# Optimization experiments

Hardware: AMD Instinct MI355X
Metric: run time of the kernel (lower is better)

## Reference

```python
import jax, jax.numpy as jnp
import numpy as np

B, S, D, H = 2, 2048, 1024, 16
HD = D // H
SCALE = HD ** -0.5
EPS = 1e-5


def setup_inputs() -> dict:
    key = jax.random.key(0)
    ks = jax.random.split(key, 12)
    s = 1.0 / np.sqrt(D)
    return {
        "query": jax.random.normal(ks[0], (B, S, D), jnp.float32),
        "key_": jax.random.normal(ks[1], (B, S, D), jnp.float32),
        "value": jax.random.normal(ks[2], (B, S, D), jnp.float32),
        "Wq": jax.random.normal(ks[3], (D, D), jnp.float32) * s,
        "bq": jnp.zeros((D,), jnp.float32),
        "Wk": jax.random.normal(ks[4], (D, D), jnp.float32) * s,
        "bk": jnp.zeros((D,), jnp.float32),
        "Wv": jax.random.normal(ks[5], (D, D), jnp.float32) * s,
        "bv": jnp.zeros((D,), jnp.float32),
        "Wo": jax.random.normal(ks[6], (D, D), jnp.float32) * s,
        "bo": jnp.zeros((D,), jnp.float32),
        "gamma": jnp.ones((D,), jnp.float32),
        "beta": jnp.zeros((D,), jnp.float32),
    }


def _split_heads(x):
    # [B,S,D] -> [B,H,S,HD]
    return x.reshape(B, S, H, HD).transpose(0, 2, 1, 3)


def reference(query, key_, value, Wq, bq, Wk, bk, Wv, bv, Wo, bo, gamma, beta):
    q = _split_heads(query @ Wq + bq)
    k = _split_heads(key_ @ Wk + bk)
    v = _split_heads(value @ Wv + bv)
    # [B,H,S,S] attention scores
    scores = jnp.einsum("bhqd,bhkd->bhqk", q, k) * SCALE
    probs = jax.nn.softmax(scores, axis=-1)  # dropout is identity in eval
    attn = jnp.einsum("bhqk,bhkd->bhqd", probs, v)
    attn = attn.transpose(0, 2, 1, 3).reshape(B, S, D)
    attn = attn @ Wo + bo
    # residual + LayerNorm
    x = query + attn
    mu = jnp.mean(x, axis=-1, keepdims=True)
    var = jnp.mean(jnp.square(x - mu), axis=-1, keepdims=True)
    out = (x - mu) * jax.lax.rsqrt(var + EPS) * gamma + beta
    return out
```

## Files before the change

kernel.cpp:

```cpp
#include <hip/hip_runtime.h>
#include <hip/hip_bf16.h>

#define DEVI __device__ __forceinline__

constexpr int Bb  = 2;
constexpr int Ss  = 2048;
constexpr int Dd  = 1024;
constexpr int Hh  = 16;
constexpr int HDh = 64;
constexpr int Mr  = Bb * Ss;
constexpr float kEps = 1e-5f;
constexpr float kQScale = 0.18033688011112043f;

typedef unsigned short u16;
typedef unsigned int   u32;
typedef u16 u16x8 __attribute__((ext_vector_type(8)));
typedef u16 u16x4 __attribute__((ext_vector_type(4)));
typedef __attribute__((ext_vector_type(8)))  short s16x8;
typedef __attribute__((ext_vector_type(16))) float f32x16;
typedef __attribute__((ext_vector_type(4)))  u32   u32x4;

DEVI float bf2f(u16 u) {
  return __builtin_bit_cast(float, ((unsigned int)u) << 16);
}
DEVI u16 f2bf(float f) {
  unsigned int x = __builtin_bit_cast(unsigned int, f);
  return (u16)((x + 0x7FFFu + ((x >> 16) & 1u)) >> 16);
}
DEVI u32 cvt_pk_bf16(float a, float b) {
  u32 r;
  asm("v_cvt_pk_bf16_f32 %0, %1, %2" : "=v"(r) : "v"(a), "v"(b));
  return r;
}
DEVI float vexp2(float x) {
  float r;
  asm("v_exp_f32 %0, %1" : "=v"(r) : "v"(x));
  return r;
}

DEVI void gload_lds16(const void* g, void* l) {
  __builtin_amdgcn_global_load_lds(
      (const __attribute__((address_space(1))) unsigned int*)(unsigned long long)(size_t)g,
      (__attribute__((address_space(3))) unsigned int*)(unsigned int)(size_t)l,
      16, 0, 0);
}


__global__ __launch_bounds__(256) void pack_all_fm(
    const float* __restrict__ X0, const float* __restrict__ X1,
    const float* __restrict__ X2,
    const float* __restrict__ W0, const float* __restrict__ W1,
    const float* __restrict__ W2, const float* __restrict__ W3,
    u16* __restrict__ Y0, u16* __restrict__ Y1, u16* __restrict__ Y2,
    u16* __restrict__ WfmBase) {
  __shared__ u16 Tl[64 * 64];
  const int t   = threadIdx.x;
  const int gid = blockIdx.x;
  if (gid < 3072) {
    const int z   = gid >> 10;
    const int rem = gid & 1023;
    const int r0  = (rem >> 4) * 64, k0 = (rem & 15) * 64;
    const float* X = z == 0 ? X0 : z == 1 ? X1 : X2;
    u16*         Y = z == 0 ? Y0 : z == 1 ? Y1 : Y2;
#pragma unroll
    for (int i = 0; i < 4; ++i) {
      const int idx = t + i * 256;
      const int r = idx >> 4, c4 = (idx & 15) << 2;
      const float4 v = *(const float4*)(X + (size_t)(r0 + r) * 1024 + k0 + c4);
      u16x4 p;
      p[0] = f2bf(v.x); p[1] = f2bf(v.y); p[2] = f2bf(v.z); p[3] = f2bf(v.w);
      *(u16x4*)&Tl[r * 64 + (c4 ^ (8 * (r & 7)))] = p;
    }
    __syncthreads();
#pragma unroll
    for (int i = 0; i < 2; ++i) {
      const int slot = t + i * 256;
      const int f = slot >> 6, l = slot & 63;
      const int l31 = l & 31, g2 = l >> 5;
      const int r = (f >> 2) * 32 + l31;
      const int c = (f & 3) * 16 + g2 * 8;
      const u16x8 v = *(const u16x8*)&Tl[r * 64 + (c ^ (8 * (r & 7)))];
      const size_t t32 = (size_t)(r0 >> 5) + (f >> 2);
      const int s = (k0 >> 4) + (f & 3);
      *(u16x8*)(Y + (t32 * 64 + s) * 512 + l * 8) = v;
    }
  } else {
    const int wz  = (gid - 3072) >> 8;
    const int rem = (gid - 3072) & 255;
    const int n0  = (rem >> 4) * 64, k0 = (rem & 15) * 64;
    const float* W = wz == 0 ? W0 : wz == 1 ? W1 : wz == 2 ? W2 : W3;
    u16* out = WfmBase + (size_t)wz * 1024 * 1024;
#pragma unroll
    for (int i = 0; i < 4; ++i) {
      const int idx = t + i * 256;
      const int r = idx >> 4, c4 = (idx & 15) << 2;
      const float4 v = *(const float4*)(W + (size_t)(k0 + r) * 1024 + n0 + c4);
      u16x4 p;
      p[0] = f2bf(v.x); p[1] = f2bf(v.y); p[2] = f2bf(v.z); p[3] = f2bf(v.w);
      *(u16x4*)&Tl[r * 64 + (c4 ^ (8 * (r & 7)))] = p;
    }
    __syncthreads();
#pragma unroll
    for (int i = 0; i < 2; ++i) {
      const int slot = t + i * 256;
      const int f = slot >> 6, l = slot & 63;
      const int l31 = l & 31, g2 = l >> 5;
      const int rbase = (f & 3) * 16 + g2 * 8;
      const int c = (f >> 2) * 32 + l31;
      u16x8 o;
#pragma unroll
      for (int j = 0; j < 8; ++j) {
        const int r = rbase + j;
        o[j] = Tl[r * 64 + (((c & ~3) ^ (8 * (r & 7))) | (c & 3))];
      }
      const size_t n32 = (size_t)(n0 >> 5) + (f >> 2);
      const int s = (k0 >> 4) + (f & 3);
      *(u16x8*)(out + (n32 * 64 + s) * 512 + l * 8) = o;
    }
  }
}

template <int MODE>
__global__ __launch_bounds__(256, 2) void gemm_reg_k(
    const u16* __restrict__ A0, const u16* __restrict__ A1,
    const u16* __restrict__ Wt0, const u16* __restrict__ Wt1,
    const float* b0, const float* b1, void* C0, void* C1,
    float e0, float e1) {
  constexpr int K = 1024, N = 1024;
  const int z = blockIdx.z;
  const u16*   A    = z ? A1 : A0;
  const u16*   Wt   = z ? Wt1 : Wt0;
  const float* bias = z ? b1 : b0;
  void*        Cv   = z ? C1 : C0;
  const float  esc  = z ? e1 : e0;

  const int t = threadIdx.x;
  const int lane = t & 63, w = t >> 6;
  const int l31 = lane & 31, g2 = lane >> 5;
  const int id  = blockIdx.y * 8 + blockIdx.x;
  const int sid = (id & 7) * 32 + (id >> 3);
  const int m0 = (sid >> 3) * 128, n0 = (sid & 7) * 128;
  const int wr = w >> 1, wc = w & 1;

  const u16* a0p = A  + ((size_t)(m0 >> 5) + 2 * wr) * 32768 + lane * 8;
  const u16* a1p = a0p + 32768;
  const u16* w0p = Wt + ((size_t)(n0 >> 5) + 2 * wc) * 32768 + lane * 8;
  const u16* w1p = w0p + 32768;

  f32x16 acc00, acc01, acc10, acc11;
#pragma unroll
  for (int r = 0; r < 16; ++r) { acc00[r] = 0.f; acc01[r] = 0.f; acc10[r] = 0.f; acc11[r] = 0.f; }

  s16x8 X[8], Y[8], Z[8];
  auto loadset = [&](s16x8* R, int k0) {
    const int o = (k0 >> 4) * 512;
    R[0] = *(const s16x8*)(a0p + o);  R[1] = *(const s16x8*)(a0p + o + 512);
    R[2] = *(const s16x8*)(a1p + o);  R[3] = *(const s16x8*)(a1p + o + 512);
    R[4] = *(const s16x8*)(w0p + o);  R[5] = *(const s16x8*)(w0p + o + 512);
    R[6] = *(const s16x8*)(w1p + o);  R[7] = *(const s16x8*)(w1p + o + 512);
  };
  auto compute = [&](const s16x8* R) {
#pragma unroll
    for (int s = 0; s < 2; ++s) {
      if constexpr (MODE == 1) {
        acc00 = __builtin_amdgcn_mfma_f32_32x32x16_bf16(R[0 + s], R[4 + s], acc00, 0, 0, 0);
        acc01 = __builtin_amdgcn_mfma_f32_32x32x16_bf16(R[0 + s], R[6 + s], acc01, 0, 0, 0);
        acc10 = __builtin_amdgcn_mfma_f32_32x32x16_bf16(R[2 + s], R[4 + s], acc10, 0, 0, 0);
        acc11 = __builtin_amdgcn_mfma_f32_32x32x16_bf16(R[2 + s], R[6 + s], acc11, 0, 0, 0);
      } else {
        acc00 = __builtin_amdgcn_mfma_f32_32x32x16_bf16(R[4 + s], R[0 + s], acc00, 0, 0, 0);
        acc01 = __builtin_amdgcn_mfma_f32_32x32x16_bf16(R[4 + s], R[2 + s], acc01, 0, 0, 0);
        acc10 = __builtin_amdgcn_mfma_f32_32x32x16_bf16(R[6 + s], R[0 + s], acc10, 0, 0, 0);
        acc11 = __builtin_amdgcn_mfma_f32_32x32x16_bf16(R[6 + s], R[2 + s], acc11, 0, 0, 0);
      }
    }
  };

  loadset(X, 0); loadset(Y, 32); loadset(Z, 64);
  int k = 0;
  for (int it = 0; it < 9; ++it, k += 96) {
    compute(X); loadset(X, k + 96);
    compute(Y); loadset(Y, k + 128);
    compute(Z); loadset(Z, k + 160);
  }
  compute(X); loadset(X, 960);
  compute(Y); loadset(Y, 992);
  compute(Z);
  compute(X);
  compute(Y);

  if constexpr (MODE == 1) {
    auto storeV = [&](const f32x16& a, int i, int j) {
      const int n = n0 + (2 * wc + j) * 32 + l31;
      const float bn = bias[n];
      u16* vout = (u16*)Cv + ((size_t)(m0 >> 11)) * (1024 * 2048) + (size_t)n * 2048 +
                  (m0 & 2047) + (2 * wr + i) * 32;
#pragma unroll
      for (int c = 0; c < 4; ++c) {
        u16x4 o;
#pragma unroll
        for (int rr = 0; rr < 4; ++rr) o[rr] = f2bf(a[4 * c + rr] + bn);
        *(u16x4*)(vout + 8 * c + 4 * g2) = o;
      }
    };
    storeV(acc00, 0, 0); storeV(acc01, 0, 1); storeV(acc10, 1, 0); storeV(acc11, 1, 1);
  } else {
    auto storeNM = [&](const f32x16& a, int i, int j) {
      const int m = m0 + (2 * wr + j) * 32 + l31;
#pragma unroll
      for (int c = 0; c < 4; ++c) {
        const int nb = n0 + (2 * wc + i) * 32 + 8 * c + 4 * g2;
        const float4 b4 = *(const float4*)&bias[nb];
        u16x4 o;
        o[0] = f2bf((a[4 * c + 0] + b4.x) * esc); o[1] = f2bf((a[4 * c + 1] + b4.y) * esc);
        o[2] = f2bf((a[4 * c + 2] + b4.z) * esc); o[3] = f2bf((a[4 * c + 3] + b4.w) * esc);
        *(u16x4*)((u16*)Cv + (size_t)m * N + nb) = o;
      }
    };
    storeNM(acc00, 0, 0); storeNM(acc01, 0, 1); storeNM(acc10, 1, 0); storeNM(acc11, 1, 1);
  }
}

__global__ __launch_bounds__(256, 2) void flash_mfma_k(
    const u16* __restrict__ Qb, const u16* __restrict__ Kb,
    const u16* __restrict__ Vtg, u16* __restrict__ Ofm) {
  __shared__ u16 smem[24576];
  const int t    = threadIdx.x;
  const int lane = t & 63;
  const int w    = t >> 6;
  const int l31  = lane & 31, g2 = lane >> 5;
  const int hid = (blockIdx.z * 16 + blockIdx.y) * 16 + blockIdx.x;
  const int sid = (hid & 7) * 64 + (hid >> 3);
  const int h = (sid >> 4) & 15, b = sid >> 8;
  const int q0 = (sid & 15) * 128 + w * 32;

  s16x8 qf0, qf1, qf2, qf3;
  {
    const u16* qp = Qb + ((size_t)(b * Ss + q0 + l31)) * Dd + h * HDh + 8 * g2;
    qf0 = *(const s16x8*)(qp);
    qf1 = *(const s16x8*)(qp + 16);
    qf2 = *(const s16x8*)(qp + 32);
    qf3 = *(const s16x8*)(qp + 48);
  }

  f32x16 accO0, accO1, zacc;
#pragma unroll
  for (int r = 0; r < 16; ++r) { accO0[r] = 0.f; accO1[r] = 0.f; zacc[r] = 0.f; }
  float l_run = 0.f;

  const int f0 = 2 * w, f1 = 2 * w + 1;
  const u16* kg0 = Kb + ((size_t)(b * Ss + 32 * (f0 >> 2) + l31)) * Dd + h * HDh + 16 * (f0 & 3) + 8 * g2;
  const u16* kg1 = Kb + ((size_t)(b * Ss + 32 * (f1 >> 2) + l31)) * Dd + h * HDh + 16 * (f1 & 3) + 8 * g2;
  const u16* vg0 = Vtg + ((size_t)((b * Hh + h) * HDh + 32 * (f0 >> 2) + l31)) * Ss + 16 * (f0 & 3) + 8 * g2;
  const u16* vg1 = Vtg + ((size_t)((b * Hh + h) * HDh + 32 * (f1 >> 2) + l31)) * Ss + 16 * (f1 & 3) + 8 * g2;

  auto stage = [&](int buf, int kt) {
    u16* base = &smem[buf * 8192];
    gload_lds16(kg0 + (size_t)kt * 64 * Dd, base + f0 * 512);
    gload_lds16(kg1 + (size_t)kt * 64 * Dd, base + f1 * 512);
    gload_lds16(vg0 + kt * 64, base + 4096 + f0 * 512);
    gload_lds16(vg1 + kt * 64, base + 4096 + f1 * 512);
  };

  stage(0, 0);
  stage(1, 1);

  int bi = 0;
  for (int i = 0; i < 32; ++i) {
    if (i < 31) asm volatile("s_waitcnt vmcnt(4)" ::: "memory");
    else        asm volatile("s_waitcnt vmcnt(0)" ::: "memory");
    __builtin_amdgcn_s_barrier();
    if (i + 2 < 32) {
      int sbuf = bi + 2; if (sbuf >= 3) sbuf -= 3;
      stage(sbuf, i + 2);
    }
    const u16* sb = &smem[bi * 8192];
    const int lb = lane * 8;

    f32x16 sc0, sc1;
    __builtin_amdgcn_s_setprio(1);
    {
      s16x8 ka;
      ka  = *(const s16x8*)&sb[(0 * 4 + 0) * 512 + lb];
      sc0 = __builtin_amdgcn_mfma_f32_32x32x16_bf16(ka, qf0, zacc, 0, 0, 0);
      ka  = *(const s16x8*)&sb[(0 * 4 + 1) * 512 + lb];
      sc0 = __builtin_amdgcn_mfma_f32_32x32x16_bf16(ka, qf1, sc0, 0, 0, 0);
      ka  = *(const s16x8*)&sb[(0 * 4 + 2) * 512 + lb];
      sc0 = __builtin_amdgcn_mfma_f32_32x32x16_bf16(ka, qf2, sc0, 0, 0, 0);
      ka  = *(const s16x8*)&sb[(0 * 4 + 3) * 512 + lb];
      sc0 = __builtin_amdgcn_mfma_f32_32x32x16_bf16(ka, qf3, sc0, 0, 0, 0);
    }
    __builtin_amdgcn_s_setprio(0);

    float lp = 0.f;
    u32 pw0[4][2];
#pragma unroll
    for (int c = 0; c < 4; ++c) {
      const float e0 = vexp2(sc0[4 * c + 0]);
      const float e1 = vexp2(sc0[4 * c + 1]);
      const float e2 = vexp2(sc0[4 * c + 2]);
      const float e3 = vexp2(sc0[4 * c + 3]);
      lp += (e0 + e1) + (e2 + e3);
      pw0[c][0] = cvt_pk_bf16(e0, e1);
      pw0[c][1] = cvt_pk_bf16(e2, e3);
    }

    __builtin_amdgcn_s_setprio(1);
    {
      s16x8 kb2;
      kb2 = *(const s16x8*)&sb[(1 * 4 + 0) * 512 + lb];
      sc1 = __builtin_amdgcn_mfma_f32_32x32x16_bf16(kb2, qf0, zacc, 0, 0, 0);
      kb2 = *(const s16x8*)&sb[(1 * 4 + 1) * 512 + lb];
      sc1 = __builtin_amdgcn_mfma_f32_32x32x16_bf16(kb2, qf1, sc1, 0, 0, 0);
      kb2 = *(const s16x8*)&sb[(1 * 4 + 2) * 512 + lb];
      sc1 = __builtin_amdgcn_mfma_f32_32x32x16_bf16(kb2, qf2, sc1, 0, 0, 0);
      kb2 = *(const s16x8*)&sb[(1 * 4 + 3) * 512 + lb];
      sc1 = __builtin_amdgcn_mfma_f32_32x32x16_bf16(kb2, qf3, sc1, 0, 0, 0);
    }
    __builtin_amdgcn_s_setprio(0);

#pragma unroll
    for (int s = 0; s < 2; ++s) {
      const int cb = 2 * (s & 1);
      u32 A0w = pw0[cb][0], B0w = pw0[cb + 1][0];
      u32 A1w = pw0[cb][1], B1w = pw0[cb + 1][1];
      asm("v_permlane32_swap_b32 %0, %1" : "+v"(A0w), "+v"(B0w));
      asm("v_permlane32_swap_b32 %0, %1" : "+v"(A1w), "+v"(B1w));
      u32x4 pv;
      pv[0] = A0w; pv[1] = A1w; pv[2] = B0w; pv[3] = B1w;
      const s16x8 pf = __builtin_bit_cast(s16x8, pv);
      const s16x8 v0 = *(const s16x8*)&sb[4096 + (0 * 4 + s) * 512 + lb];
      const s16x8 v1 = *(const s16x8*)&sb[4096 + (1 * 4 + s) * 512 + lb];
      __builtin_amdgcn_s_setprio(1);
      accO0 = __builtin_amdgcn_mfma_f32_32x32x16_bf16(v0, pf, accO0, 0, 0, 0);
      accO1 = __builtin_amdgcn_mfma_f32_32x32x16_bf16(v1, pf, accO1, 0, 0, 0);
      __builtin_amdgcn_s_setprio(0);
    }

    u32 pw1[4][2];
#pragma unroll
    for (int c = 0; c < 4; ++c) {
      const float e0 = vexp2(sc1[4 * c + 0]);
      const float e1 = vexp2(sc1[4 * c + 1]);
      const float e2 = vexp2(sc1[4 * c + 2]);
      const float e3 = vexp2(sc1[4 * c + 3]);
      lp += (e0 + e1) + (e2 + e3);
      pw1[c][0] = cvt_pk_bf16(e0, e1);
      pw1[c][1] = cvt_pk_bf16(e2, e3);
    }
    l_run += lp;

#pragma unroll
    for (int s = 2; s < 4; ++s) {
      const int cb = 2 * (s & 1);
      u32 A0w = pw1[cb][0], B0w = pw1[cb + 1][0];
      u32 A1w = pw1[cb][1], B1w = pw1[cb + 1][1];
      asm("v_permlane32_swap_b32 %0, %1" : "+v"(A0w), "+v"(B0w));
      asm("v_permlane32_swap_b32 %0, %1" : "+v"(A1w), "+v"(B1w));
      u32x4 pv;
      pv[0] = A0w; pv[1] = A1w; pv[2] = B0w; pv[3] = B1w;
      const s16x8 pf = __builtin_bit_cast(s16x8, pv);
      const s16x8 v0 = *(const s16x8*)&sb[4096 + (0 * 4 + s) * 512 + lb];
      const s16x8 v1 = *(const s16x8*)&sb[4096 + (1 * 4 + s) * 512 + lb];
      __builtin_amdgcn_s_setprio(1);
      accO0 = __builtin_amdgcn_mfma_f32_32x32x16_bf16(v0, pf, accO0, 0, 0, 0);
      accO1 = __builtin_amdgcn_mfma_f32_32x32x16_bf16(v1, pf, accO1, 0, 0, 0);
      __builtin_amdgcn_s_setprio(0);
    }

    bi = (bi == 2) ? 0 : bi + 1;
  }

  __syncthreads();

  const float l_tot = l_run + __shfl_xor(l_run, 32);
  const float inv = 1.f / l_tot;
  u16* Ol = &smem[w * 2304];
#pragma unroll
  for (int c = 0; c < 4; ++c) {
    u16x4 pk;
#pragma unroll
    for (int rr = 0; rr < 4; ++rr) pk[rr] = f2bf(accO0[4 * c + rr] * inv);
    *(u16x4*)&Ol[l31 * 72 + 0 * 32 + c * 8 + g2 * 4] = pk;
#pragma unroll
    for (int rr = 0; rr < 4; ++rr) pk[rr] = f2bf(accO1[4 * c + rr] * inv);
    *(u16x4*)&Ol[l31 * 72 + 1 * 32 + c * 8 + g2 * 4] = pk;
  }
  const size_t m32 = (size_t)((b * Ss + q0) >> 5);
#pragma unroll
  for (int s = 0; s < 4; ++s) {
    const u16x8 vv = *(const u16x8*)&Ol[l31 * 72 + s * 16 + g2 * 8];
    *(u16x8*)(Ofm + (m32 * 64 + h * 4 + s) * 512 + lane * 8) = vv;
  }
}

__global__ __launch_bounds__(256) void resid_ln_k(const float* __restrict__ x0,
                                                  const u16* __restrict__ x1,
                                                  const float* __restrict__ gamma,
                                                  const float* __restrict__ beta,
                                                  float* __restrict__ out) {
  const int row = blockIdx.x;
  const int t   = threadIdx.x;
  const size_t base = (size_t)row * Dd + t * 4;
  const float4 a = *(const float4*)(x0 + base);
  const u16x4  c = *(const u16x4*)(x1 + base);
  float x[4] = {a.x + bf2f(c[0]), a.y + bf2f(c[1]), a.z + bf2f(c[2]), a.w + bf2f(c[3])};
  float s  = (x[0] + x[1]) + (x[2] + x[3]);
  float s2 = fmaf(x[0], x[0], fmaf(x[1], x[1], fmaf(x[2], x[2], x[3] * x[3])));
#pragma unroll
  for (int m = 1; m < 64; m <<= 1) {
    s  += __shfl_xor(s, m);
    s2 += __shfl_xor(s2, m);
  }
  __shared__ float red[8];
  const int wave = t >> 6;
  if ((t & 63) == 0) {
    red[wave]     = s;
    red[wave + 4] = s2;
  }
  __syncthreads();
  s  = (red[0] + red[1]) + (red[2] + red[3]);
  s2 = (red[4] + red[5]) + (red[6] + red[7]);
  const float mu  = s * (1.f / Dd);
  const float var = s2 * (1.f / Dd) - mu * mu;
  const float rs  = rsqrtf(var + kEps);
  const float4 g  = *(const float4*)(gamma + t * 4);
  const float4 be = *(const float4*)(beta + t * 4);
  float4 o;
  o.x = (x[0] - mu) * rs * g.x + be.x;
  o.y = (x[1] - mu) * rs * g.y + be.y;
  o.z = (x[2] - mu) * rs * g.z + be.z;
  o.w = (x[3] - mu) * rs * g.w + be.w;
  *(float4*)(out + base) = o;
}

extern "C" void kernel_launch(void* const* d_in, const int* in_sizes, int n_in,
                              void* d_out, int out_size, void* d_ws,
                              size_t ws_size, hipStream_t stream) {
  const float* query = (const float*)d_in[0];
  const float* key_  = (const float*)d_in[1];
  const float* value = (const float*)d_in[2];
  const float* Wq = (const float*)d_in[3];
  const float* bq = (const float*)d_in[4];
  const float* Wk = (const float*)d_in[5];
  const float* bk = (const float*)d_in[6];
  const float* Wv = (const float*)d_in[7];
  const float* bv = (const float*)d_in[8];
  const float* Wo = (const float*)d_in[9];
  const float* bo = (const float*)d_in[10];
  const float* gamma = (const float*)d_in[11];
  const float* beta  = (const float*)d_in[12];
  float* out = (float*)d_out;

  char* ws = (char*)d_ws;
  u16* Xv  = (u16*)(ws + (size_t)0);
  u16* Qb  = (u16*)(ws + (size_t)0);
  u16* Kb  = (u16*)(ws + (size_t)8 * 1024 * 1024);
  u16* XoB = (u16*)(ws + (size_t)8 * 1024 * 1024);
  u16* Vtg = (u16*)(ws + (size_t)16 * 1024 * 1024);
  u16* WfB = (u16*)(ws + (size_t)24 * 1024 * 1024);
  u16* Wqf = WfB;
  u16* Wkf = WfB + (size_t)1 * 1024 * 1024;
  u16* Wvf = WfB + (size_t)2 * 1024 * 1024;
  u16* Wof = WfB + (size_t)3 * 1024 * 1024;
  u16* Xq  = (u16*)d_out;
  u16* Xk  = (u16*)d_out + (size_t)Mr * Dd;
  u16* Ofm = (u16*)d_out;

  pack_all_fm<<<4096, 256, 0, stream>>>(query, key_, value, Wq, Wk, Wv, Wo,
                                        Xq, Xk, Xv, WfB);
  gemm_reg_k<1><<<dim3(8, 32, 1), 256, 0, stream>>>(
      Xv, Xv, Wvf, Wvf, bv, bv, Vtg, Vtg, 1.f, 1.f);
  gemm_reg_k<0><<<dim3(8, 32, 2), 256, 0, stream>>>(
      Xq, Xk, Wqf, Wkf, bq, bk, Qb, Kb, kQScale, 1.f);
  flash_mfma_k<<<dim3(16, 16, 2), 256, 0, stream>>>(Qb, Kb, Vtg, Ofm);
  gemm_reg_k<0><<<dim3(8, 32, 1), 256, 0, stream>>>(
      Ofm, Ofm, Wof, Wof, bo, bo, XoB, XoB, 1.f, 1.f);
  resid_ln_k<<<Mr, 256, 0, stream>>>(query, XoB, gamma, beta, out);
}
```

Before: 127.1 us.

## Store K and V projections in fragment-major tiles for contiguous flash loads

The V and K projection GEMMs now write their outputs in a fragment-major tiled layout, so each 64-lane fragment the attention kernel stages into LDS is one contiguous 1KB block. Before, those loads used strided row addresses. The goal is fully coalesced global-to-LDS loads in the flash kernel, at the cost of scattered 8-byte stores in the GEMM epilogues. A new MODE 2 template path selects the K layout for z==1, but only for K; Q is still written row-major.

```diff
diff --git a/kernel.cpp b/kernel.cpp
--- a/kernel.cpp
+++ b/kernel.cpp
@@ -190,22 +190,25 @@
   compute(Y);
 
   if constexpr (MODE == 1) {
-    auto storeV = [&](const f32x16& a, int i, int j) {
-      const int n = n0 + (2 * wc + j) * 32 + l31;
-      const float bn = bias[n];
-      u16* vout = (u16*)Cv + ((size_t)(m0 >> 11)) * (1024 * 2048) + (size_t)n * 2048 +
-                  (m0 & 2047) + (2 * wr + i) * 32;
+    auto storeVfm = [&](const f32x16& a, int i, int j) {
+      const int nn = n0 + (2 * wc + j) * 32 + l31;
+      const float bn = bias[nn];
+      const int nnT = (n0 >> 5) + 2 * wc + j;
+      const int sb  = ((m0 & 2047) + (2 * wr + i) * 32) >> 4;
+      u16* vbase = (u16*)Cv + (size_t)(m0 >> 11) * (1024 * 2048);
 #pragma unroll
       for (int c = 0; c < 4; ++c) {
         u16x4 o;
 #pragma unroll
         for (int rr = 0; rr < 4; ++rr) o[rr] = f2bf(a[4 * c + rr] + bn);
-        *(u16x4*)(vout + 8 * c + 4 * g2) = o;
+        u16* dst = vbase + ((size_t)nnT * 128 + sb + (c >> 1)) * 512 +
+                   (l31 + 32 * (c & 1)) * 8 + 4 * g2;
+        *(u16x4*)dst = o;
       }
     };
-    storeV(acc00, 0, 0); storeV(acc01, 0, 1); storeV(acc10, 1, 0); storeV(acc11, 1, 1);
+    storeVfm(acc00, 0, 0); storeVfm(acc01, 0, 1); storeVfm(acc10, 1, 0); storeVfm(acc11, 1, 1);
   } else {
-    auto storeNM = [&](const f32x16& a, int i, int j) {
+    auto storeRow = [&](const f32x16& a, int i, int j) {
       const int m = m0 + (2 * wr + j) * 32 + l31;
 #pragma unroll
       for (int c = 0; c < 4; ++c) {
@@ -217,13 +220,32 @@
         *(u16x4*)((u16*)Cv + (size_t)m * N + nb) = o;
       }
     };
-    storeNM(acc00, 0, 0); storeNM(acc01, 0, 1); storeNM(acc10, 1, 0); storeNM(acc11, 1, 1);
+    auto storeKfm = [&](const f32x16& a, int i, int j) {
+      const int mt = (m0 >> 5) + 2 * wr + j;
+#pragma unroll
+      for (int c = 0; c < 4; ++c) {
+        const int nb = n0 + (2 * wc + i) * 32 + 8 * c + 4 * g2;
+        const float4 b4 = *(const float4*)&bias[nb];
+        u16x4 o;
+        o[0] = f2bf(a[4 * c + 0] + b4.x); o[1] = f2bf(a[4 * c + 1] + b4.y);
+        o[2] = f2bf(a[4 * c + 2] + b4.z); o[3] = f2bf(a[4 * c + 3] + b4.w);
+        const int nq = (n0 >> 4) + (2 * wc + i) * 2 + (c >> 1);
+        u16* dst = (u16*)Cv + ((size_t)mt * 64 + nq) * 512 +
+                   (l31 + 32 * (c & 1)) * 8 + 4 * g2;
+        *(u16x4*)dst = o;
+      }
+    };
+    if (MODE == 2 && z == 1) {
+      storeKfm(acc00, 0, 0); storeKfm(acc01, 0, 1); storeKfm(acc10, 1, 0); storeKfm(acc11, 1, 1);
+    } else {
+      storeRow(acc00, 0, 0); storeRow(acc01, 0, 1); storeRow(acc10, 1, 0); storeRow(acc11, 1, 1);
+    }
   }
 }
 
 __global__ __launch_bounds__(256, 2) void flash_mfma_k(
-    const u16* __restrict__ Qb, const u16* __restrict__ Kb,
-    const u16* __restrict__ Vtg, u16* __restrict__ Ofm) {
+    const u16* __restrict__ Qb, const u16* __restrict__ Kf,
+    const u16* __restrict__ Vf, u16* __restrict__ Ofm) {
   __shared__ u16 smem[24576];
   const int t    = threadIdx.x;
   const int lane = t & 63;
@@ -249,17 +271,17 @@
   float l_run = 0.f;
 
   const int f0 = 2 * w, f1 = 2 * w + 1;
-  const u16* kg0 = Kb + ((size_t)(b * Ss + 32 * (f0 >> 2) + l31)) * Dd + h * HDh + 16 * (f0 & 3) + 8 * g2;
-  const u16* kg1 = Kb + ((size_t)(b * Ss + 32 * (f1 >> 2) + l31)) * Dd + h * HDh + 16 * (f1 & 3) + 8 * g2;
-  const u16* vg0 = Vtg + ((size_t)((b * Hh + h) * HDh + 32 * (f0 >> 2) + l31)) * Ss + 16 * (f0 & 3) + 8 * g2;
-  const u16* vg1 = Vtg + ((size_t)((b * Hh + h) * HDh + 32 * (f1 >> 2) + l31)) * Ss + 16 * (f1 & 3) + 8 * g2;
+  const u16* kg0 = Kf + (((size_t)b * 64 + (f0 >> 2)) * 64 + h * 4 + (f0 & 3)) * 512 + lane * 8;
+  const u16* kg1 = Kf + (((size_t)b * 64 + (f1 >> 2)) * 64 + h * 4 + (f1 & 3)) * 512 + lane * 8;
+  const u16* vg0 = Vf + (size_t)b * 2097152 + (((size_t)h * 2 + (f0 >> 2)) * 128 + (f0 & 3)) * 512 + lane * 8;
+  const u16* vg1 = Vf + (size_t)b * 2097152 + (((size_t)h * 2 + (f1 >> 2)) * 128 + (f1 & 3)) * 512 + lane * 8;
 
   auto stage = [&](int buf, int kt) {
     u16* base = &smem[buf * 8192];
-    gload_lds16(kg0 + (size_t)kt * 64 * Dd, base + f0 * 512);
-    gload_lds16(kg1 + (size_t)kt * 64 * Dd, base + f1 * 512);
-    gload_lds16(vg0 + kt * 64, base + 4096 + f0 * 512);
-    gload_lds16(vg1 + kt * 64, base + 4096 + f1 * 512);
+    gload_lds16(kg0 + (size_t)kt * 65536, base + f0 * 512);
+    gload_lds16(kg1 + (size_t)kt * 65536, base + f1 * 512);
+    gload_lds16(vg0 + (size_t)kt * 2048, base + 4096 + f0 * 512);
+    gload_lds16(vg1 + (size_t)kt * 2048, base + 4096 + f1 * 512);
   };
 
   stage(0, 0);
@@ -455,9 +477,9 @@
   char* ws = (char*)d_ws;
   u16* Xv  = (u16*)(ws + (size_t)0);
   u16* Qb  = (u16*)(ws + (size_t)0);
-  u16* Kb  = (u16*)(ws + (size_t)8 * 1024 * 1024);
+  u16* Kf  = (u16*)(ws + (size_t)8 * 1024 * 1024);
   u16* XoB = (u16*)(ws + (size_t)8 * 1024 * 1024);
-  u16* Vtg = (u16*)(ws + (size_t)16 * 1024 * 1024);
+  u16* Vf  = (u16*)(ws + (size_t)16 * 1024 * 1024);
   u16* WfB = (u16*)(ws + (size_t)24 * 1024 * 1024);
   u16* Wqf = WfB;
   u16* Wkf = WfB + (size_t)1 * 1024 * 1024;
@@ -470,10 +492,10 @@
   pack_all_fm<<<4096, 256, 0, stream>>>(query, key_, value, Wq, Wk, Wv, Wo,
                                         Xq, Xk, Xv, WfB);
   gemm_reg_k<1><<<dim3(8, 32, 1), 256, 0, stream>>>(
-      Xv, Xv, Wvf, Wvf, bv, bv, Vtg, Vtg, 1.f, 1.f);
-  gemm_reg_k<0><<<dim3(8, 32, 2), 256, 0, stream>>>(
-      Xq, Xk, Wqf, Wkf, bq, bk, Qb, Kb, kQScale, 1.f);
-  flash_mfma_k<<<dim3(16, 16, 2), 256, 0, stream>>>(Qb, Kb, Vtg, Ofm);
+      Xv, Xv, Wvf, Wvf, bv, bv, Vf, Vf, 1.f, 1.f);
+  gemm_reg_k<2><<<dim3(8, 32, 2), 256, 0, stream>>>(
+      Xq, Xk, Wqf, Wkf, bq, bk, Qb, Kf, kQScale, 1.f);
+  flash_mfma_k<<<dim3(16, 16, 2), 256, 0, stream>>>(Qb, Kf, Vf, Ofm);
   gemm_reg_k<0><<<dim3(8, 32, 1), 256, 0, stream>>>(
       Ofm, Ofm, Wof, Wof, bo, bo, XoB, XoB, 1.f, 1.f);
   resid_ln_k<<<Mr, 256, 0, stream>>>(query, XoB, gamma, beta, out);
```

New measurement: 125.6 us. No clear change (-1.2%).
